# Kernel optimization log

Hardware: AMD Instinct MI355X
Metric: run time of the kernel (lower is better)

The kernel has to match this reference:

```python
import jax, jax.numpy as jnp
import numpy as np

B, DEC, ENC, H = 4, 128, 512, 768


def setup_inputs() -> dict:
    key = jax.random.key(0)
    k1, k2, k3, k4, k5 = jax.random.split(key, 5)
    scale = 1.0 / np.sqrt(H)
    return {
        "decoder_state": jax.random.normal(k1, (B, DEC, H), dtype=jnp.float32),
        "encoder_outputs": jax.random.normal(k2, (B, ENC, H), dtype=jnp.float32),
        "mask": jnp.zeros((B, DEC, ENC), dtype=jnp.float32),
        # Learned params: torch nn.Linear(H, H, bias=False) weights, stored as (in, out)
        "W1": jax.random.normal(k3, (H, H), dtype=jnp.float32) * scale,
        "W2": jax.random.normal(k4, (H, H), dtype=jnp.float32) * scale,
        "vt": jax.random.normal(k5, (H,), dtype=jnp.float32) * scale,
    }


def reference(decoder_state, encoder_outputs, mask, W1, W2, vt):
    # enc_t: (B, enc, H), dec_t: (B, dec, H)
    enc_t = jnp.einsum("beh,hk->bek", encoder_outputs, W1)
    dec_t = jnp.einsum("bdh,hk->bdk", decoder_state, W2)
    # Bahdanau additive score: tanh of broadcast sum -> (B, dec, enc, H), reduce with vt
    hidden = jnp.tanh(enc_t[:, None, :, :] + dec_t[:, :, None, :])
    log_score = jnp.einsum("bdek,k->bde", hidden, vt)
    log_score_masked = log_score + mask
    return (log_score_masked, log_score)
```

## Files before the change

### kernel.cpp

```cpp
#include <hip/hip_runtime.h>
#include <hip/hip_bf16.h>

#define B_SZ   4
#define DEC_SZ 128
#define ENC_SZ 512
#define H_SZ   768
#define OUT_N  (B_SZ * DEC_SZ * ENC_SZ)

typedef __attribute__((ext_vector_type(8))) short s8v;
typedef __attribute__((ext_vector_type(4))) float fvec4;

__device__ inline unsigned short f2bf(float x) {
  union { float f; unsigned u; } v; v.f = x;
  unsigned r = v.u + 0x7FFF + ((v.u >> 16) & 1);
  return (unsigned short)(r >> 16);
}

__device__ inline s8v load8(const unsigned short* p) { return *(const s8v*)p; }
__device__ inline s8v load8(const float* p) {
  float4 a = ((const float4*)p)[0];
  float4 b = ((const float4*)p)[1];
  unsigned short r[8] = {f2bf(a.x), f2bf(a.y), f2bf(a.z), f2bf(a.w),
                         f2bf(b.x), f2bf(b.y), f2bf(b.z), f2bf(b.w)};
  return *(const s8v*)r;
}

__global__ __launch_bounds__(256) void transpose_w(const float* __restrict__ W1,
                                                   const float* __restrict__ W2,
                                                   unsigned short* __restrict__ T1,
                                                   unsigned short* __restrict__ T2) {
  const float* W = blockIdx.z ? W2 : W1;
  unsigned short* T = blockIdx.z ? T2 : T1;
  __shared__ float tile[64][65];
  int c0 = blockIdx.x * 64;
  int r0 = blockIdx.y * 64;
  int tx = threadIdx.x & 63, ty = threadIdx.x >> 6;
#pragma unroll
  for (int i = 0; i < 16; ++i) {
    int r = ty + i * 4;
    tile[r][tx] = W[(size_t)(r0 + r) * H_SZ + c0 + tx];
  }
  __syncthreads();
#pragma unroll
  for (int i = 0; i < 16; ++i) {
    int c = ty + i * 4;
    T[(size_t)(c0 + c) * H_SZ + r0 + tx] = f2bf(tile[tx][c]);
  }
}

template <bool TILED, typename TA, typename TB>
__device__ inline void gemm_body(const TA* __restrict__ A, const TB* __restrict__ B,
                                 float* __restrict__ C, int ldc, int bx, int by) {
  const int m0 = bx * 128;
  const int n0 = by * 64;

  __shared__ unsigned short As[128][40];
  __shared__ unsigned short Bs[64][40];

  const int tid  = threadIdx.x;
  const int wave = tid >> 6;
  const int lane = tid & 63;
  const int l16  = lane & 15;
  const int quad = lane >> 4;
  const int wm   = wave * 32;

  int ar[2], ak[2];
#pragma unroll
  for (int i = 0; i < 2; ++i) {
    int seg = tid + 256 * i;
    ar[i] = seg >> 2; ak[i] = (seg & 3) * 8;
  }
  const int br = tid >> 2, bk = (tid & 3) * 8;

  fvec4 acc[2][4];
#pragma unroll
  for (int i = 0; i < 2; ++i)
#pragma unroll
    for (int j = 0; j < 4; ++j) acc[i][j] = (fvec4)0.f;

  s8v pa[2], pb;
#pragma unroll
  for (int i = 0; i < 2; ++i) pa[i] = load8(A + (size_t)(m0 + ar[i]) * H_SZ + ak[i]);
  pb = load8(B + (size_t)(n0 + br) * H_SZ + bk);

  for (int k0 = 0; k0 < H_SZ; k0 += 32) {
    __syncthreads();
#pragma unroll
    for (int i = 0; i < 2; ++i) *(s8v*)&As[ar[i]][ak[i]] = pa[i];
    *(s8v*)&Bs[br][bk] = pb;
    __syncthreads();

    if (k0 + 32 < H_SZ) {
#pragma unroll
      for (int i = 0; i < 2; ++i)
        pa[i] = load8(A + (size_t)(m0 + ar[i]) * H_SZ + k0 + 32 + ak[i]);
      pb = load8(B + (size_t)(n0 + br) * H_SZ + k0 + 32 + bk);
    }

    s8v af[2], bf[4];
#pragma unroll
    for (int i = 0; i < 2; ++i) af[i] = *(const s8v*)&As[wm + i * 16 + l16][quad * 8];
#pragma unroll
    for (int j = 0; j < 4; ++j) bf[j] = *(const s8v*)&Bs[j * 16 + l16][quad * 8];
#pragma unroll
    for (int i = 0; i < 2; ++i)
#pragma unroll
      for (int j = 0; j < 4; ++j)
        acc[i][j] = __builtin_amdgcn_mfma_f32_16x16x32_bf16(af[i], bf[j], acc[i][j], 0, 0, 0);
  }

  const float C2 = 2.885390082f;
#pragma unroll
  for (int i = 0; i < 2; ++i) {
    int mbase = m0 + wm + i * 16 + quad * 4;
#pragma unroll
    for (int j = 0; j < 4; ++j) {
      int n = n0 + j * 16 + l16;
      if (TILED) {
        float4 o;
        o.x = __builtin_amdgcn_exp2f(acc[i][j][0] * C2);
        o.y = __builtin_amdgcn_exp2f(acc[i][j][1] * C2);
        o.z = __builtin_amdgcn_exp2f(acc[i][j][2] * C2);
        o.w = __builtin_amdgcn_exp2f(acc[i][j][3] * C2);
        int bIdx = n >> 9, es = (n >> 6) & 7, el = n & 63;
        ((float4*)C)[((size_t)(bIdx * 8 + es) * 192 + (mbase >> 2)) * 64 + el] = o;
      } else {
#pragma unroll
        for (int r = 0; r < 4; ++r)
          C[(size_t)(mbase + r) * ldc + n] = __builtin_amdgcn_exp2f(acc[i][j][r] * C2);
      }
    }
  }
}

__global__ __launch_bounds__(256) void gemm_both(const unsigned short* __restrict__ W1T,
                                                 const float* __restrict__ enc,
                                                 const float* __restrict__ dec,
                                                 const unsigned short* __restrict__ W2T,
                                                 float* __restrict__ peT,
                                                 float* __restrict__ pdm) {
  int bid = blockIdx.x;
  if (bid < 192) {
    gemm_body<true>(W1T, enc, peT, 0, bid % 6, bid / 6);
  } else {
    int r = bid - 192;
    gemm_body<false>(dec, W2T, pdm, H_SZ, r % 4, r / 4);
  }
}

__global__ __launch_bounds__(256) void score_out(const float* __restrict__ peT,
                                                 const float* __restrict__ pdm,
                                                 const float* __restrict__ vt,
                                                 const float* __restrict__ mask,
                                                 float* __restrict__ out) {
  const int tid  = threadIdx.x;
  const int lane = tid & 63;
  const int wave = __builtin_amdgcn_readfirstlane(tid >> 6);

  const int L    = blockIdx.x;
  const int xcd  = L & 7;
  const int slot = L >> 3;
  const int col  = xcd + 8 * (slot & 3);
  const int b    = col >> 3;
  const int es   = col & 7;
  const int d    = (slot >> 2) * 4 + wave;

  float sumv = 0.f;
#pragma unroll
  for (int j = 0; j < 12; ++j) sumv += vt[lane + 64 * j];
#pragma unroll
  for (int s = 1; s < 64; s <<= 1) sumv += __shfl_xor(sumv, s, 64);

  const float* pdrow = pdm + (size_t)(b * DEC_SZ + d) * H_SZ;
  const float4* pe4 = (const float4*)peT + (size_t)col * 192 * 64 + lane;

  float t0 = 0.f, t1 = 0.f;
  float4 buf[12];
#pragma unroll
  for (int i = 0; i < 12; ++i) buf[i] = pe4[(size_t)i * 64];

#pragma unroll 12
  for (int c = 0; c < 192; ++c) {
    float4 cur = buf[c % 12];
    if (c + 12 < 192) buf[c % 12] = pe4[(size_t)(c + 12) * 64];
    float4 v4 = *(const float4*)(vt + c * 4);
    float4 p4 = *(const float4*)(pdrow + c * 4);
    t0 = fmaf(v4.x, __builtin_amdgcn_rcpf(fmaf(cur.x, p4.x, 1.f)), t0);
    t1 = fmaf(v4.y, __builtin_amdgcn_rcpf(fmaf(cur.y, p4.y, 1.f)), t1);
    t0 = fmaf(v4.z, __builtin_amdgcn_rcpf(fmaf(cur.z, p4.z, 1.f)), t0);
    t1 = fmaf(v4.w, __builtin_amdgcn_rcpf(fmaf(cur.w, p4.w, 1.f)), t1);
  }
  float t = t0 + t1;

  const int e = es * 64 + lane;
  size_t idx = ((size_t)(b * DEC_SZ + d)) * ENC_SZ + e;
  float s = fmaf(-2.f, t, sumv);
  out[idx] = s + mask[idx];
  out[OUT_N + idx] = s;
}

extern "C" void kernel_launch(void* const* d_in, const int* in_sizes, int n_in,
                              void* d_out, int out_size, void* d_ws, size_t ws_size,
                              hipStream_t stream) {
  (void)in_sizes; (void)n_in; (void)out_size; (void)ws_size;
  const float* dec  = (const float*)d_in[0];
  const float* enc  = (const float*)d_in[1];
  const float* mask = (const float*)d_in[2];
  const float* W1   = (const float*)d_in[3];
  const float* W2   = (const float*)d_in[4];
  const float* vt   = (const float*)d_in[5];
  float* out = (float*)d_out;

  float* peT = (float*)d_ws;
  float* pdm = peT + (size_t)H_SZ * B_SZ * ENC_SZ;
  unsigned short* W1T = (unsigned short*)(pdm + (size_t)B_SZ * DEC_SZ * H_SZ);
  unsigned short* W2T = W1T + (size_t)H_SZ * H_SZ;

  transpose_w<<<dim3(12, 12, 2), 256, 0, stream>>>(W1, W2, W1T, W2T);
  gemm_both<<<dim3(240), 256, 0, stream>>>(W1T, enc, dec, W2T, peT, pdm);
  score_out<<<dim3(1024), 256, 0, stream>>>(peT, pdm, vt, mask, out);
}
```

Baseline: 134.0 us.

## Split H reduction across waves and merge four reciprocals into one

```diff
diff --git a/kernel.cpp b/kernel.cpp
--- a/kernel.cpp
+++ b/kernel.cpp
@@ -148,7 +148,7 @@
   }
 }
 
-__global__ __launch_bounds__(256) void score_out(const float* __restrict__ peT,
+__global__ __launch_bounds__(512) void score_out(const float* __restrict__ peT,
                                                  const float* __restrict__ pdm,
                                                  const float* __restrict__ vt,
                                                  const float* __restrict__ mask,
@@ -156,6 +156,8 @@
   const int tid  = threadIdx.x;
   const int lane = tid & 63;
   const int wave = __builtin_amdgcn_readfirstlane(tid >> 6);
+  const int dw   = wave & 3;
+  const int kh   = wave >> 2;
 
   const int L    = blockIdx.x;
   const int xcd  = L & 7;
@@ -163,7 +165,7 @@
   const int col  = xcd + 8 * (slot & 3);
   const int b    = col >> 3;
   const int es   = col & 7;
-  const int d    = (slot >> 2) * 4 + wave;
+  const int d    = (slot >> 2) * 4 + dw;
 
   float sumv = 0.f;
 #pragma unroll
@@ -171,32 +173,44 @@
 #pragma unroll
   for (int s = 1; s < 64; s <<= 1) sumv += __shfl_xor(sumv, s, 64);
 
-  const float* pdrow = pdm + (size_t)(b * DEC_SZ + d) * H_SZ;
-  const float4* pe4 = (const float4*)peT + (size_t)col * 192 * 64 + lane;
-
-  float t0 = 0.f, t1 = 0.f;
-  float4 buf[12];
-#pragma unroll
-  for (int i = 0; i < 12; ++i) buf[i] = pe4[(size_t)i * 64];
-
-#pragma unroll 12
-  for (int c = 0; c < 192; ++c) {
-    float4 cur = buf[c % 12];
-    if (c + 12 < 192) buf[c % 12] = pe4[(size_t)(c + 12) * 64];
-    float4 v4 = *(const float4*)(vt + c * 4);
+  const float* pdrow = pdm + (size_t)(b * DEC_SZ + d) * H_SZ + kh * 384;
+  const float* vth   = vt + kh * 384;
+  const float4* pe4  = (const float4*)peT + ((size_t)col * 192 + kh * 96) * 64 + lane;
+
+  float t0 = 0.f;
+  float4 buf[8];
+#pragma unroll
+  for (int i = 0; i < 8; ++i) buf[i] = pe4[(size_t)i * 64];
+
+#pragma unroll 8
+  for (int c = 0; c < 96; ++c) {
+    float4 cur = buf[c & 7];
+    if (c + 8 < 96) buf[c & 7] = pe4[(size_t)(c + 8) * 64];
+    float4 v4 = *(const float4*)(vth + c * 4);
     float4 p4 = *(const float4*)(pdrow + c * 4);
-    t0 = fmaf(v4.x, __builtin_amdgcn_rcpf(fmaf(cur.x, p4.x, 1.f)), t0);
-    t1 = fmaf(v4.y, __builtin_amdgcn_rcpf(fmaf(cur.y, p4.y, 1.f)), t1);
-    t0 = fmaf(v4.z, __builtin_amdgcn_rcpf(fmaf(cur.z, p4.z, 1.f)), t0);
-    t1 = fmaf(v4.w, __builtin_amdgcn_rcpf(fmaf(cur.w, p4.w, 1.f)), t1);
-  }
-  float t = t0 + t1;
-
-  const int e = es * 64 + lane;
-  size_t idx = ((size_t)(b * DEC_SZ + d)) * ENC_SZ + e;
-  float s = fmaf(-2.f, t, sumv);
-  out[idx] = s + mask[idx];
-  out[OUT_N + idx] = s;
+    float a  = fmaf(cur.x, p4.x, 1.f);
+    float bq = fmaf(cur.y, p4.y, 1.f);
+    float cq = fmaf(cur.z, p4.z, 1.f);
+    float dq = fmaf(cur.w, p4.w, 1.f);
+    float ab = a * bq, cd = cq * dq;
+    float n01 = fmaf(v4.x, bq, v4.y * a);
+    float n23 = fmaf(v4.z, dq, v4.w * cq);
+    float num = fmaf(n23, ab, n01 * cd);
+    float r = __builtin_amdgcn_rcpf(ab * cd);
+    t0 = fmaf(num, r, t0);
+  }
+
+  __shared__ float tred[4][64];
+  if (kh) tred[dw][lane] = t0;
+  __syncthreads();
+  if (!kh) {
+    float t = t0 + tred[dw][lane];
+    const int e = es * 64 + lane;
+    size_t idx = ((size_t)(b * DEC_SZ + d)) * ENC_SZ + e;
+    float s = fmaf(-2.f, t, sumv);
+    out[idx] = s + mask[idx];
+    out[OUT_N + idx] = s;
+  }
 }
 
 extern "C" void kernel_launch(void* const* d_in, const int* in_sizes, int n_in,
@@ -218,5 +232,5 @@
 
   transpose_w<<<dim3(12, 12, 2), 256, 0, stream>>>(W1, W2, W1T, W2T);
   gemm_both<<<dim3(240), 256, 0, stream>>>(W1T, enc, dec, W2T, peT, pdm);
-  score_out<<<dim3(1024), 256, 0, stream>>>(peT, pdm, vt, mask, out);
-}
+  score_out<<<dim3(1024), 512, 0, stream>>>(peT, pdm, vt, mask, out);
+}
```

Result: faster. 127.6 us, median of 2 (-4.8%).
